# Optimization experiments

Hardware: AMD Instinct MI355X
Metric: run time of the kernel (lower is better)

## Reference

```python
import jax, jax.numpy as jnp
import numpy as np


def setup_inputs() -> dict:
    key = jax.random.key(0)
    k1, k2 = jax.random.split(key)
    B, C, Tx, Ty, d = 16, 64, 128, 128, 768
    xs = jax.random.normal(k1, (B, Tx, d), dtype=jnp.float32)
    ys = jax.random.normal(k2, (B, C, Ty, d), dtype=jnp.float32)
    return {"xs": xs, "ys": ys}


def reference(xs, ys):
    """UnifiedRetriever HardAttention scoring.

    xs: (B, T_x, d) mention poly-code embeddings
    ys: (B, C, T_y, d) candidate entity poly-code embeddings
    returns: (B, C) scores
    Matches torch: matmul(xs, ys.reshape(B,-1,d).T).reshape(B,Tx,C,Ty).max(-1)[0].sum(1)
    """
    # (B, Tx, C, Ty) dot-product similarity scores
    scores = jnp.einsum("bxd,bcyd->bxcy", xs, ys)
    # max over candidate tokens, sum over mention tokens -> (B, C)
    return scores.max(axis=-1).sum(axis=1)
```

## Files before the change

kernel.cpp:

```cpp
#include <hip/hip_runtime.h>

#define NB 16
#define NC 64
#define TX 128
#define TY 128
#define DD 768
#define BK 64
#define NT (DD / BK)

typedef __bf16 bf16_t;
typedef __bf16 bf16x8 __attribute__((ext_vector_type(8)));
typedef __bf16 bf16x4 __attribute__((ext_vector_type(4)));
typedef float  f32x4  __attribute__((ext_vector_type(4)));

__device__ __forceinline__ unsigned swz(unsigned r, unsigned byte) {
  return r * 128u + ((((byte >> 4) & 7u) ^ (r & 7u)) << 4) + (byte & 15u);
}

__device__ __forceinline__ void cvt_store(void* dst, f32x4 v) {
  bf16x4 q;
  q[0] = (bf16_t)v[0]; q[1] = (bf16_t)v[1]; q[2] = (bf16_t)v[2]; q[3] = (bf16_t)v[3];
  *(bf16x4*)dst = q;
}

__global__ __launch_bounds__(512, 2) void ur_score_kernel(
    const float* __restrict__ xs, const float* __restrict__ ys,
    float* __restrict__ out)
{
  __shared__ char lds[2][2][16384];
  __shared__ float wsum[8];

  const int u  = blockIdx.x;
  const int b  = u & 15;
  const int c  = u >> 4;
  const int bc = b * NC + c;

  const int tid  = threadIdx.x;
  const int lane = tid & 63;
  const int w    = tid >> 6;

  const unsigned r0 = (unsigned)tid >> 4;
  const unsigned j0 = (unsigned)tid & 15u;
  const unsigned soff0 = swz(r0, j0 * 8u);
  const float* Ap = xs + (size_t)b  * TX * DD + r0 * DD + j0 * 4;
  const float* Bp = ys + (size_t)bc * TY * DD + r0 * DD + j0 * 4;

  f32x4 acc[8];
  #pragma unroll
  for (int n = 0; n < 8; ++n)
    #pragma unroll
    for (int k = 0; k < 4; ++k)
      acc[n][k] = 0.0f;

  f32x4 pa[4], pb[4];

  #pragma unroll
  for (int i = 0; i < 4; ++i) {
    pa[i] = *(const f32x4*)(Ap + i * 32 * DD);
    pb[i] = __builtin_nontemporal_load((const f32x4*)(Bp + i * 32 * DD));
  }
  #pragma unroll
  for (int i = 0; i < 4; ++i) {
    cvt_store(&lds[0][0][soff0 + 4096u * i], pa[i]);
    cvt_store(&lds[0][1][soff0 + 4096u * i], pb[i]);
  }
  #pragma unroll
  for (int i = 0; i < 4; ++i) {
    pa[i] = *(const f32x4*)(Ap + BK + i * 32 * DD);
    pb[i] = __builtin_nontemporal_load((const f32x4*)(Bp + BK + i * 32 * DD));
  }
  asm volatile("s_waitcnt lgkmcnt(0)" ::: "memory");
  __builtin_amdgcn_s_barrier();
  asm volatile("" ::: "memory");

  const unsigned kb = ((unsigned)lane >> 4) << 4;
  const unsigned rA = (unsigned)(w * 16 + (lane & 15));
  const unsigned rB = (unsigned)(lane & 15);
  const unsigned aoff0 = swz(rA, kb),      aoff1 = swz(rA, 64u + kb);
  const unsigned boff0 = swz(rB, kb),      boff1 = swz(rB, 64u + kb);

  int cur = 0;
  for (int t = 0; t < NT; ++t) {
    if (t + 1 < NT) {
      #pragma unroll
      for (int i = 0; i < 4; ++i) {
        cvt_store(&lds[cur ^ 1][0][soff0 + 4096u * i], pa[i]);
        cvt_store(&lds[cur ^ 1][1][soff0 + 4096u * i], pb[i]);
      }
    }
    if (t + 2 < NT) {
      #pragma unroll
      for (int i = 0; i < 4; ++i) {
        pa[i] = *(const f32x4*)(Ap + (t + 2) * BK + i * 32 * DD);
        pb[i] = __builtin_nontemporal_load((const f32x4*)(Bp + (t + 2) * BK + i * 32 * DD));
      }
    }
    {
      bf16x8 af0 = *(const bf16x8*)&lds[cur][0][aoff0];
      bf16x8 bfr[8];
      #pragma unroll
      for (int n = 0; n < 8; ++n)
        bfr[n] = *(const bf16x8*)&lds[cur][1][boff0 + 2048u * n];
      #pragma unroll
      for (int n = 0; n < 8; ++n)
        acc[n] = __builtin_amdgcn_mfma_f32_16x16x32_bf16(af0, bfr[n], acc[n], 0, 0, 0);
    }
    {
      bf16x8 af1 = *(const bf16x8*)&lds[cur][0][aoff1];
      bf16x8 bfr[8];
      #pragma unroll
      for (int n = 0; n < 8; ++n)
        bfr[n] = *(const bf16x8*)&lds[cur][1][boff1 + 2048u * n];
      #pragma unroll
      for (int n = 0; n < 8; ++n)
        acc[n] = __builtin_amdgcn_mfma_f32_16x16x32_bf16(af1, bfr[n], acc[n], 0, 0, 0);
    }

    asm volatile("s_waitcnt lgkmcnt(0)" ::: "memory");
    __builtin_amdgcn_s_barrier();
    asm volatile("" ::: "memory");
    cur ^= 1;
  }

  float rm[4];
  #pragma unroll
  for (int i = 0; i < 4; ++i) {
    float v = acc[0][i];
    #pragma unroll
    for (int n = 1; n < 8; ++n) v = fmaxf(v, acc[n][i]);
    rm[i] = v;
  }
  #pragma unroll
  for (int mask = 1; mask < 16; mask <<= 1)
    #pragma unroll
    for (int i = 0; i < 4; ++i)
      rm[i] = fmaxf(rm[i], __shfl_xor(rm[i], mask, 64));

  float ps = rm[0] + rm[1] + rm[2] + rm[3];
  ps += __shfl_xor(ps, 16, 64);
  ps += __shfl_xor(ps, 32, 64);

  if (lane == 0) wsum[w] = ps;
  __syncthreads();
  if (tid == 0) {
    float s = 0.0f;
    #pragma unroll
    for (int i = 0; i < 8; ++i) s += wsum[i];
    out[bc] = s;
  }
}

extern "C" void kernel_launch(void* const* d_in, const int* in_sizes, int n_in,
                              void* d_out, int out_size, void* d_ws, size_t ws_size,
                              hipStream_t stream) {
  const float* xs = (const float*)d_in[0];
  const float* ys = (const float*)d_in[1];
  float* out = (float*)d_out;
  ur_score_kernel<<<dim3(NB * NC), dim3(512), 0, stream>>>(xs, ys, out);
}
```

Baseline: 75.91 us.

## Load A fragments directly from global into registers, bypassing LDS

Each wave now loads its own 16-row A (xs) fragment straight from global memory into registers and converts it to bf16, instead of staging xs through shared memory. This halves LDS usage and removes the A LDS stores and reads. The B store and prefetch are moved after the MFMAs to overlap with compute. The cost is a shorter A prefetch distance (one tile instead of two), so global-load latency is less hidden, plus uncoalesced strided A loads.

```diff
diff --git a/kernel.cpp b/kernel.cpp
--- a/kernel.cpp
+++ b/kernel.cpp
@@ -23,11 +23,18 @@
   *(bf16x4*)dst = q;
 }
 
+__device__ __forceinline__ bf16x8 cvt8(f32x4 lo, f32x4 hi) {
+  bf16x8 q;
+  q[0] = (bf16_t)lo[0]; q[1] = (bf16_t)lo[1]; q[2] = (bf16_t)lo[2]; q[3] = (bf16_t)lo[3];
+  q[4] = (bf16_t)hi[0]; q[5] = (bf16_t)hi[1]; q[6] = (bf16_t)hi[2]; q[7] = (bf16_t)hi[3];
+  return q;
+}
+
 __global__ __launch_bounds__(512, 2) void ur_score_kernel(
     const float* __restrict__ xs, const float* __restrict__ ys,
     float* __restrict__ out)
 {
-  __shared__ char lds[2][2][16384];
+  __shared__ char lds[2][16384];
   __shared__ float wsum[8];
 
   const int u  = blockIdx.x;
@@ -42,8 +49,11 @@
   const unsigned r0 = (unsigned)tid >> 4;
   const unsigned j0 = (unsigned)tid & 15u;
   const unsigned soff0 = swz(r0, j0 * 8u);
-  const float* Ap = xs + (size_t)b  * TX * DD + r0 * DD + j0 * 4;
   const float* Bp = ys + (size_t)bc * TY * DD + r0 * DD + j0 * 4;
+
+  const unsigned arow = (unsigned)(w * 16 + (lane & 15));
+  const unsigned ak   = ((unsigned)(lane >> 4)) << 3;
+  const float* Afp = xs + (size_t)b * TX * DD + arow * DD + ak;
 
   f32x4 acc[8];
   #pragma unroll
@@ -52,70 +62,69 @@
     for (int k = 0; k < 4; ++k)
       acc[n][k] = 0.0f;
 
-  f32x4 pa[4], pb[4];
+  f32x4 pb[4];
+  f32x4 afp0, afp1, afp2, afp3;
 
+  afp0 = *(const f32x4*)(Afp + 0);
+  afp1 = *(const f32x4*)(Afp + 4);
+  afp2 = *(const f32x4*)(Afp + 32);
+  afp3 = *(const f32x4*)(Afp + 36);
   #pragma unroll
-  for (int i = 0; i < 4; ++i) {
-    pa[i] = *(const f32x4*)(Ap + i * 32 * DD);
+  for (int i = 0; i < 4; ++i)
     pb[i] = __builtin_nontemporal_load((const f32x4*)(Bp + i * 32 * DD));
-  }
   #pragma unroll
-  for (int i = 0; i < 4; ++i) {
-    cvt_store(&lds[0][0][soff0 + 4096u * i], pa[i]);
-    cvt_store(&lds[0][1][soff0 + 4096u * i], pb[i]);
-  }
+  for (int i = 0; i < 4; ++i)
+    cvt_store(&lds[0][soff0 + 4096u * i], pb[i]);
   #pragma unroll
-  for (int i = 0; i < 4; ++i) {
-    pa[i] = *(const f32x4*)(Ap + BK + i * 32 * DD);
+  for (int i = 0; i < 4; ++i)
     pb[i] = __builtin_nontemporal_load((const f32x4*)(Bp + BK + i * 32 * DD));
-  }
   asm volatile("s_waitcnt lgkmcnt(0)" ::: "memory");
   __builtin_amdgcn_s_barrier();
   asm volatile("" ::: "memory");
 
   const unsigned kb = ((unsigned)lane >> 4) << 4;
-  const unsigned rA = (unsigned)(w * 16 + (lane & 15));
   const unsigned rB = (unsigned)(lane & 15);
-  const unsigned aoff0 = swz(rA, kb),      aoff1 = swz(rA, 64u + kb);
-  const unsigned boff0 = swz(rB, kb),      boff1 = swz(rB, 64u + kb);
+  const unsigned boff0 = swz(rB, kb), boff1 = swz(rB, 64u + kb);
 
   int cur = 0;
   for (int t = 0; t < NT; ++t) {
+    bf16x8 af0 = cvt8(afp0, afp1);
+    bf16x8 af1 = cvt8(afp2, afp3);
     if (t + 1 < NT) {
-      #pragma unroll
-      for (int i = 0; i < 4; ++i) {
-        cvt_store(&lds[cur ^ 1][0][soff0 + 4096u * i], pa[i]);
-        cvt_store(&lds[cur ^ 1][1][soff0 + 4096u * i], pb[i]);
-      }
-    }
-    if (t + 2 < NT) {
-      #pragma unroll
-      for (int i = 0; i < 4; ++i) {
-        pa[i] = *(const f32x4*)(Ap + (t + 2) * BK + i * 32 * DD);
-        pb[i] = __builtin_nontemporal_load((const f32x4*)(Bp + (t + 2) * BK + i * 32 * DD));
-      }
+      const float* An = Afp + (t + 1) * BK;
+      afp0 = *(const f32x4*)(An + 0);
+      afp1 = *(const f32x4*)(An + 4);
+      afp2 = *(const f32x4*)(An + 32);
+      afp3 = *(const f32x4*)(An + 36);
     }
     {
-      bf16x8 af0 = *(const bf16x8*)&lds[cur][0][aoff0];
       bf16x8 bfr[8];
       #pragma unroll
       for (int n = 0; n < 8; ++n)
-        bfr[n] = *(const bf16x8*)&lds[cur][1][boff0 + 2048u * n];
+        bfr[n] = *(const bf16x8*)&lds[cur][boff0 + 2048u * n];
       #pragma unroll
       for (int n = 0; n < 8; ++n)
         acc[n] = __builtin_amdgcn_mfma_f32_16x16x32_bf16(af0, bfr[n], acc[n], 0, 0, 0);
     }
     {
-      bf16x8 af1 = *(const bf16x8*)&lds[cur][0][aoff1];
       bf16x8 bfr[8];
       #pragma unroll
       for (int n = 0; n < 8; ++n)
-        bfr[n] = *(const bf16x8*)&lds[cur][1][boff1 + 2048u * n];
+        bfr[n] = *(const bf16x8*)&lds[cur][boff1 + 2048u * n];
       #pragma unroll
       for (int n = 0; n < 8; ++n)
         acc[n] = __builtin_amdgcn_mfma_f32_16x16x32_bf16(af1, bfr[n], acc[n], 0, 0, 0);
     }
-
+    if (t + 1 < NT) {
+      #pragma unroll
+      for (int i = 0; i < 4; ++i)
+        cvt_store(&lds[cur ^ 1][soff0 + 4096u * i], pb[i]);
+    }
+    if (t + 2 < NT) {
+      #pragma unroll
+      for (int i = 0; i < 4; ++i)
+        pb[i] = __builtin_nontemporal_load((const f32x4*)(Bp + (t + 2) * BK + i * 32 * DD));
+    }
     asm volatile("s_waitcnt lgkmcnt(0)" ::: "memory");
     __builtin_amdgcn_s_barrier();
     asm volatile("" ::: "memory");
```

Result: slower. 80.78 us (+6.4%).

## Split candidate tokens across two blocks and combine partial maxima in a second kernel

Applied to the files above, without the earlier changes.

Each (b,c) pair is now handled by two blocks, each covering half of the Ty rows. The halves write per-row partial maxima to workspace, and a small combine kernel takes the max of the two halves and sums over Tx. The goal is twice as many blocks with a smaller per-block footprint, raising occupancy and parallelism. The cost is reloading and reconverting xs twice as often, an extra kernel launch, and a workspace round trip. The original single-kernel path remains as a fallback when the workspace is too small.

```diff
diff --git a/kernel.cpp b/kernel.cpp
--- a/kernel.cpp
+++ b/kernel.cpp
@@ -23,6 +23,141 @@
   *(bf16x4*)dst = q;
 }
 
+__global__ __launch_bounds__(512, 3) void ur_half_kernel(
+    const float* __restrict__ xs, const float* __restrict__ ys,
+    float* __restrict__ pmax)
+{
+  __shared__ char ldsA[2][16384];
+  __shared__ char ldsB[2][8192];
+
+  const int u  = blockIdx.x;
+  const int b  = u & 15;
+  const int h  = (u >> 4) & 1;
+  const int c  = u >> 5;
+  const int bc = b * NC + c;
+
+  const int tid  = threadIdx.x;
+  const int lane = tid & 63;
+  const int w    = tid >> 6;
+
+  const unsigned r0 = (unsigned)tid >> 4;
+  const unsigned j0 = (unsigned)tid & 15u;
+  const unsigned soff = swz(r0, j0 * 8u);
+  const float* Ap = xs + (size_t)b  * TX * DD + r0 * DD + j0 * 4;
+  const float* Bp = ys + (size_t)bc * TY * DD + (size_t)(h * 64 + r0) * DD + j0 * 4;
+
+  f32x4 acc[4];
+  #pragma unroll
+  for (int n = 0; n < 4; ++n)
+    #pragma unroll
+    for (int k = 0; k < 4; ++k)
+      acc[n][k] = 0.0f;
+
+  f32x4 pa[4], pb[2];
+
+  #pragma unroll
+  for (int i = 0; i < 4; ++i)
+    pa[i] = *(const f32x4*)(Ap + i * 32 * DD);
+  #pragma unroll
+  for (int i = 0; i < 2; ++i)
+    pb[i] = __builtin_nontemporal_load((const f32x4*)(Bp + i * 32 * DD));
+  #pragma unroll
+  for (int i = 0; i < 4; ++i)
+    cvt_store(&ldsA[0][soff + 4096u * i], pa[i]);
+  #pragma unroll
+  for (int i = 0; i < 2; ++i)
+    cvt_store(&ldsB[0][soff + 4096u * i], pb[i]);
+  #pragma unroll
+  for (int i = 0; i < 4; ++i)
+    pa[i] = *(const f32x4*)(Ap + BK + i * 32 * DD);
+  #pragma unroll
+  for (int i = 0; i < 2; ++i)
+    pb[i] = __builtin_nontemporal_load((const f32x4*)(Bp + BK + i * 32 * DD));
+  asm volatile("s_waitcnt lgkmcnt(0)" ::: "memory");
+  __builtin_amdgcn_s_barrier();
+  asm volatile("" ::: "memory");
+
+  const unsigned kb = ((unsigned)lane >> 4) << 4;
+  const unsigned rA = (unsigned)(w * 16 + (lane & 15));
+  const unsigned rB = (unsigned)(lane & 15);
+  const unsigned aoff0 = swz(rA, kb), aoff1 = swz(rA, 64u + kb);
+  const unsigned boff0 = swz(rB, kb), boff1 = swz(rB, 64u + kb);
+
+  int cur = 0;
+  for (int t = 0; t < NT; ++t) {
+    if (t + 1 < NT) {
+      #pragma unroll
+      for (int i = 0; i < 4; ++i)
+        cvt_store(&ldsA[cur ^ 1][soff + 4096u * i], pa[i]);
+      #pragma unroll
+      for (int i = 0; i < 2; ++i)
+        cvt_store(&ldsB[cur ^ 1][soff + 4096u * i], pb[i]);
+    }
+    if (t + 2 < NT) {
+      #pragma unroll
+      for (int i = 0; i < 4; ++i)
+        pa[i] = *(const f32x4*)(Ap + (t + 2) * BK + i * 32 * DD);
+      #pragma unroll
+      for (int i = 0; i < 2; ++i)
+        pb[i] = __builtin_nontemporal_load((const f32x4*)(Bp + (t + 2) * BK + i * 32 * DD));
+    }
+    {
+      bf16x8 af = *(const bf16x8*)&ldsA[cur][aoff0];
+      bf16x8 bfr[4];
+      #pragma unroll
+      for (int n = 0; n < 4; ++n)
+        bfr[n] = *(const bf16x8*)&ldsB[cur][boff0 + 2048u * n];
+      #pragma unroll
+      for (int n = 0; n < 4; ++n)
+        acc[n] = __builtin_amdgcn_mfma_f32_16x16x32_bf16(af, bfr[n], acc[n], 0, 0, 0);
+    }
+    {
+      bf16x8 af = *(const bf16x8*)&ldsA[cur][aoff1];
+      bf16x8 bfr[4];
+      #pragma unroll
+      for (int n = 0; n < 4; ++n)
+        bfr[n] = *(const bf16x8*)&ldsB[cur][boff1 + 2048u * n];
+      #pragma unroll
+      for (int n = 0; n < 4; ++n)
+        acc[n] = __builtin_amdgcn_mfma_f32_16x16x32_bf16(af, bfr[n], acc[n], 0, 0, 0);
+    }
+    asm volatile("s_waitcnt lgkmcnt(0)" ::: "memory");
+    __builtin_amdgcn_s_barrier();
+    asm volatile("" ::: "memory");
+    cur ^= 1;
+  }
+
+  float rm[4];
+  #pragma unroll
+  for (int i = 0; i < 4; ++i)
+    rm[i] = fmaxf(fmaxf(acc[0][i], acc[1][i]), fmaxf(acc[2][i], acc[3][i]));
+  #pragma unroll
+  for (int mask = 1; mask < 16; mask <<= 1)
+    #pragma unroll
+    for (int i = 0; i < 4; ++i)
+      rm[i] = fmaxf(rm[i], __shfl_xor(rm[i], mask, 64));
+
+  if ((lane & 15) == 0) {
+    float* p = pmax + ((size_t)(bc * 2 + h)) * 128 + w * 16 + (lane >> 4) * 4;
+    #pragma unroll
+    for (int i = 0; i < 4; ++i) p[i] = rm[i];
+  }
+}
+
+__global__ __launch_bounds__(256) void ur_comb_kernel(
+    const float* __restrict__ pmax, float* __restrict__ out)
+{
+  const int gw   = blockIdx.x * 4 + (threadIdx.x >> 6);
+  const int lane = threadIdx.x & 63;
+  const float* p0 = pmax + (size_t)gw * 256;
+  const float* p1 = p0 + 128;
+  float v = fmaxf(p0[lane], p1[lane]) + fmaxf(p0[lane + 64], p1[lane + 64]);
+  #pragma unroll
+  for (int mask = 1; mask < 64; mask <<= 1)
+    v += __shfl_xor(v, mask, 64);
+  if (lane == 0) out[gw] = v;
+}
+
 __global__ __launch_bounds__(512, 2) void ur_score_kernel(
     const float* __restrict__ xs, const float* __restrict__ ys,
     float* __restrict__ out)
@@ -76,8 +211,8 @@
   const unsigned kb = ((unsigned)lane >> 4) << 4;
   const unsigned rA = (unsigned)(w * 16 + (lane & 15));
   const unsigned rB = (unsigned)(lane & 15);
-  const unsigned aoff0 = swz(rA, kb),      aoff1 = swz(rA, 64u + kb);
-  const unsigned boff0 = swz(rB, kb),      boff1 = swz(rB, 64u + kb);
+  const unsigned aoff0 = swz(rA, kb), aoff1 = swz(rA, 64u + kb);
+  const unsigned boff0 = swz(rB, kb), boff1 = swz(rB, 64u + kb);
 
   int cur = 0;
   for (int t = 0; t < NT; ++t) {
@@ -115,7 +250,6 @@
       for (int n = 0; n < 8; ++n)
         acc[n] = __builtin_amdgcn_mfma_f32_16x16x32_bf16(af1, bfr[n], acc[n], 0, 0, 0);
     }
-
     asm volatile("s_waitcnt lgkmcnt(0)" ::: "memory");
     __builtin_amdgcn_s_barrier();
     asm volatile("" ::: "memory");
@@ -156,5 +290,12 @@
   const float* xs = (const float*)d_in[0];
   const float* ys = (const float*)d_in[1];
   float* out = (float*)d_out;
-  ur_score_kernel<<<dim3(NB * NC), dim3(512), 0, stream>>>(xs, ys, out);
-}
+  const size_t need = (size_t)NB * NC * 2 * 128 * sizeof(float);
+  if (ws_size >= need) {
+    float* pmax = (float*)d_ws;
+    ur_half_kernel<<<dim3(NB * NC * 2), dim3(512), 0, stream>>>(xs, ys, pmax);
+    ur_comb_kernel<<<dim3(NB * NC / 4), dim3(256), 0, stream>>>(pmax, out);
+  } else {
+    ur_score_kernel<<<dim3(NB * NC), dim3(512), 0, stream>>>(xs, ys, out);
+  }
+}
```

After: 100.1 us. 1.32x slower.
